# Performance work log

Hardware: AMD Instinct MI355X
Metric: run time of the kernel (lower is better)

## Reference

```python
import jax, jax.numpy as jnp
import numpy as np
import math

IN_CH = 256
RED_CH = 32  # max(256//8, 32)

def setup_inputs() -> dict:
    key = jax.random.key(0)
    k1, k2, k3, k4, k5 = jax.random.split(key, 5)
    x = jax.random.normal(k1, (2, IN_CH, 8, 28, 28), dtype=jnp.float32)
    # 1x1x1 Conv3d weights, kaiming-normal style scale (fan_out)
    def kaiming(k, shape):
        fan_out = shape[0]
        std = math.sqrt(2.0 / fan_out)
        return jax.random.normal(k, shape, dtype=jnp.float32) * std
    q_w = kaiming(k2, (RED_CH, IN_CH))
    k_w = kaiming(k3, (RED_CH, IN_CH))
    v_w = kaiming(k4, (RED_CH, IN_CH))
    out_w = kaiming(k5, (IN_CH, RED_CH))
    return {"x": x, "q_w": q_w, "k_w": k_w, "v_w": v_w, "out_w": out_w}

def reference(x, q_w, k_w, v_w, out_w):
    b, c, t, h, w = x.shape
    n = t * h * w
    xf = x.reshape(b, c, n)  # [B, C, N] (1x1x1 conv == channel matmul)
    q = jnp.einsum('rc,bcn->brn', q_w, xf)  # [B, Cr, N]
    k = jnp.einsum('rc,bcn->brn', k_w, xf)
    v = jnp.einsum('rc,bcn->brn', v_w, xf)
    scale = 1.0 / math.sqrt(RED_CH)
    attn = jnp.einsum('bri,brj->bij', q, k) * scale  # [B, N, N]
    attn = jax.nn.softmax(attn, axis=2)
    out = jnp.einsum('brj,bij->bri', v, attn)  # [B, Cr, N]
    out = jnp.einsum('cr,brn->bcn', out_w, out).reshape(b, c, t, h, w)
    return x + out
```

## Files before the change

### kernel.cpp

```cpp
#include <hip/hip_runtime.h>
#include <hip/hip_bf16.h>

#define NPOS 6272
#define NT   98
#define CIN  256
#define CR   32
#define BATCH 2
#define QS2  0.25503371989518595f
#define PPITCH 72

typedef short bf16x8s __attribute__((ext_vector_type(8)));
typedef short short4v __attribute__((ext_vector_type(4)));
typedef float f32x4   __attribute__((ext_vector_type(4)));
typedef unsigned short ushort_t;

__device__ __forceinline__ ushort_t f2bf(float f) {
    unsigned u = __builtin_bit_cast(unsigned, f);
    u += 0x7fff + ((u >> 16) & 1);
    return (ushort_t)(u >> 16);
}
__device__ __forceinline__ float bf2f(ushort_t h) {
    return __builtin_bit_cast(float, (unsigned)h << 16);
}

__global__ __launch_bounds__(256, 4) void qkv_kernel(
    const float* __restrict__ x, const float* __restrict__ qw,
    const float* __restrict__ kw, const float* __restrict__ vw,
    ushort_t* __restrict__ Qh, ushort_t* __restrict__ Ql,
    ushort_t* __restrict__ Kh, ushort_t* __restrict__ Kl,
    ushort_t* __restrict__ Vt)
{
    const int b   = blockIdx.y;
    const int z   = blockIdx.z;
    const int nl  = threadIdx.x & 63;
    const int n   = blockIdx.x * 64 + nl;
    const int g   = __builtin_amdgcn_readfirstlane(threadIdx.x >> 6);
    const float* w  = (z == 0) ? qw : (z == 1) ? kw : vw;
    const float* wr = w + g * 8 * CIN;
    const float* xb = x + (size_t)b * CIN * NPOS + n;

    float acc[8];
#pragma unroll
    for (int i = 0; i < 8; ++i) acc[i] = 0.f;
#pragma unroll 2
    for (int cb = 0; cb < CIN; cb += 16) {
        float xv[16];
#pragma unroll
        for (int i = 0; i < 16; ++i)
            xv[i] = xb[(size_t)(cb + i) * NPOS];
#pragma unroll
        for (int i = 0; i < 16; ++i)
#pragma unroll
            for (int r = 0; r < 8; ++r)
                acc[r] += wr[r * CIN + cb + i] * xv[i];
    }
    if (z == 2) {
#pragma unroll
        for (int i = 0; i < 8; ++i)
            Vt[((size_t)b * CR + g * 8 + i) * NPOS + n] = f2bf(acc[i]);
    } else {
        ushort_t* dh = (z == 0) ? Qh : Kh;
        ushort_t* dl = (z == 0) ? Ql : Kl;
        float s = (z == 0) ? QS2 : 1.0f;
        bf16x8s fh, fl;
#pragma unroll
        for (int i = 0; i < 8; ++i) {
            float v = acc[i] * s;
            ushort_t h = f2bf(v);
            fh[i] = (short)h;
            fl[i] = (short)f2bf(v - bf2f(h));
        }
        size_t off = ((size_t)b * NPOS + n) * CR + g * 8;
        *(bf16x8s*)(dh + off) = fh;
        *(bf16x8s*)(dl + off) = fl;
    }
}

template <int ITERS>
__global__ __launch_bounds__(128, 3) void attn_kernel(
    const ushort_t* __restrict__ Qh, const ushort_t* __restrict__ Ql,
    const ushort_t* __restrict__ Kh, const ushort_t* __restrict__ Kl,
    const ushort_t* __restrict__ Vt, ushort_t* __restrict__ Opart,
    float* __restrict__ Mp, float* __restrict__ Lp)
{
    __shared__ __align__(16) ushort_t pbuf[2 * 2 * 16 * PPITCH];

    const int lane = threadIdx.x & 63;
    const int wv   = threadIdx.x >> 6;
    const int col  = lane & 15;
    const int quad = lane >> 4;
    const int b    = blockIdx.z;
    const int s    = blockIdx.y;
    const int qw0  = blockIdx.x * 64 + wv * 32;
    ushort_t* pb   = &pbuf[wv * 2 * 16 * PPITCH];

    const ushort_t* Qhb = Qh + (size_t)b * NPOS * CR;
    const ushort_t* Qlb = Ql + (size_t)b * NPOS * CR;
    const ushort_t* Khb = Kh + (size_t)b * NPOS * CR;
    const ushort_t* Klb = Kl + (size_t)b * NPOS * CR;
    const ushort_t* Vtb = Vt + (size_t)b * CR * NPOS;

    bf16x8s qbh[2], qbl[2];
    qbh[0] = *(const bf16x8s*)(Qhb + (size_t)(qw0 + col) * CR + quad * 8);
    qbh[1] = *(const bf16x8s*)(Qhb + (size_t)(qw0 + 16 + col) * CR + quad * 8);
    qbl[0] = *(const bf16x8s*)(Qlb + (size_t)(qw0 + col) * CR + quad * 8);
    qbl[1] = *(const bf16x8s*)(Qlb + (size_t)(qw0 + 16 + col) * CR + quad * 8);

    f32x4 oc[2][2];
#pragma unroll
    for (int h = 0; h < 2; ++h)
#pragma unroll
        for (int c = 0; c < 2; ++c)
#pragma unroll
            for (int r = 0; r < 4; ++r) oc[h][c][r] = 0.f;
    float m_[2] = { -1e30f, -1e30f };
    float l_[2] = { 0.f, 0.f };

#pragma unroll 7
    for (int it = 0; it < ITERS; ++it) {
        const int j0 = (s * ITERS + it) * 64;
        bf16x8s kh[4], kl[4], vb[2][2];
#pragma unroll
        for (int f = 0; f < 4; ++f) {
            kh[f] = *(const bf16x8s*)(Khb + (size_t)(j0 + f * 16 + col) * CR + quad * 8);
            kl[f] = *(const bf16x8s*)(Klb + (size_t)(j0 + f * 16 + col) * CR + quad * 8);
        }
#pragma unroll
        for (int k2 = 0; k2 < 2; ++k2)
#pragma unroll
            for (int c = 0; c < 2; ++c)
                vb[k2][c] = *(const bf16x8s*)(Vtb + (size_t)(c * 16 + col) * NPOS
                                              + j0 + k2 * 32 + quad * 8);

        f32x4 z4; z4[0] = 0.f; z4[1] = 0.f; z4[2] = 0.f; z4[3] = 0.f;
#pragma unroll
        for (int h = 0; h < 2; ++h) {
            f32x4 sc[4];
#pragma unroll
            for (int f = 0; f < 4; ++f) {
                sc[f] = __builtin_amdgcn_mfma_f32_16x16x32_bf16(kl[f], qbh[h], z4, 0, 0, 0);
                sc[f] = __builtin_amdgcn_mfma_f32_16x16x32_bf16(kh[f], qbl[h], sc[f], 0, 0, 0);
                sc[f] = __builtin_amdgcn_mfma_f32_16x16x32_bf16(kh[f], qbh[h], sc[f], 0, 0, 0);
            }
            float v0 = fmaxf(fmaxf(sc[0][0], sc[0][1]), fmaxf(sc[0][2], sc[0][3]));
            float v1 = fmaxf(fmaxf(sc[1][0], sc[1][1]), fmaxf(sc[1][2], sc[1][3]));
            float v2 = fmaxf(fmaxf(sc[2][0], sc[2][1]), fmaxf(sc[2][2], sc[2][3]));
            float v3 = fmaxf(fmaxf(sc[3][0], sc[3][1]), fmaxf(sc[3][2], sc[3][3]));
            float v  = fmaxf(fmaxf(v0, v1), fmaxf(v2, v3));
            v = fmaxf(v, __shfl_xor(v, 16));
            v = fmaxf(v, __shfl_xor(v, 32));
            float mo = m_[h];
            float mn = fmaxf(mo, v);
            float al = __builtin_amdgcn_exp2f(mo - mn);
            float lsum = 0.f;
#pragma unroll
            for (int f = 0; f < 4; ++f) {
                float p0 = __builtin_amdgcn_exp2f(sc[f][0] - mn);
                float p1 = __builtin_amdgcn_exp2f(sc[f][1] - mn);
                float p2 = __builtin_amdgcn_exp2f(sc[f][2] - mn);
                float p3 = __builtin_amdgcn_exp2f(sc[f][3] - mn);
                lsum += (p0 + p1) + (p2 + p3);
                short4v pk;
                pk[0] = (short)f2bf(p0); pk[1] = (short)f2bf(p1);
                pk[2] = (short)f2bf(p2); pk[3] = (short)f2bf(p3);
                *(short4v*)(&pb[h * 16 * PPITCH + col * PPITCH + f * 16 + quad * 4]) = pk;
            }
            m_[h] = mn;
            l_[h] = l_[h] * al + lsum;
#pragma unroll
            for (int r = 0; r < 4; ++r) { oc[h][0][r] *= al; oc[h][1][r] *= al; }
        }
#pragma unroll
        for (int h = 0; h < 2; ++h) {
#pragma unroll
            for (int k2 = 0; k2 < 2; ++k2) {
                bf16x8s pbo = *(const bf16x8s*)(
                    &pb[h * 16 * PPITCH + col * PPITCH + k2 * 32 + quad * 8]);
                oc[h][0] = __builtin_amdgcn_mfma_f32_16x16x32_bf16(vb[k2][0], pbo, oc[h][0], 0, 0, 0);
                oc[h][1] = __builtin_amdgcn_mfma_f32_16x16x32_bf16(vb[k2][1], pbo, oc[h][1], 0, 0, 0);
            }
        }
    }

#pragma unroll
    for (int h = 0; h < 2; ++h) {
        float l = l_[h];
        l += __shfl_xor(l, 16);
        l += __shfl_xor(l, 32);
        l_[h] = l;
    }

    const size_t sb = (size_t)(s * BATCH + b);
    ushort_t* Ob = Opart + sb * CR * NPOS;
#pragma unroll
    for (int h = 0; h < 2; ++h)
#pragma unroll
        for (int c = 0; c < 2; ++c)
#pragma unroll
            for (int r = 0; r < 4; ++r) {
                int ch = c * 16 + quad * 4 + r;
                Ob[(size_t)ch * NPOS + qw0 + h * 16 + col] = f2bf(oc[h][c][r]);
            }
    if (quad == 0) {
#pragma unroll
        for (int h = 0; h < 2; ++h) {
            Mp[sb * NPOS + qw0 + h * 16 + col] = m_[h];
            Lp[sb * NPOS + qw0 + h * 16 + col] = l_[h];
        }
    }
}

template <int S_>
__global__ __launch_bounds__(256) void merge_kernel(
    const ushort_t* __restrict__ Opart, const float* __restrict__ Mp,
    const float* __restrict__ Lp, float* __restrict__ Omrg)
{
    const int b  = blockIdx.y;
    const int z  = blockIdx.z;
    const int nl = threadIdx.x & 63;
    const int n  = blockIdx.x * 64 + nl;
    const int g  = __builtin_amdgcn_readfirstlane(threadIdx.x >> 6);
    const int r  = z * 4 + g;

    float mg = -1e30f;
#pragma unroll
    for (int s = 0; s < S_; ++s)
        mg = fmaxf(mg, Mp[(size_t)(s * BATCH + b) * NPOS + n]);
    float lg = 0.f, acc = 0.f;
#pragma unroll
    for (int s = 0; s < S_; ++s) {
        size_t sb = (size_t)(s * BATCH + b);
        float w = __builtin_amdgcn_exp2f(Mp[sb * NPOS + n] - mg);
        lg  += w * Lp[sb * NPOS + n];
        acc += w * bf2f(Opart[(sb * CR + r) * NPOS + n]);
    }
    Omrg[((size_t)b * CR + r) * NPOS + n] = acc / lg;
}

__global__ __launch_bounds__(256) void proj_kernel(
    const float* __restrict__ Omrg, const float* __restrict__ ow,
    const float* __restrict__ x, float* __restrict__ y)
{
    const int b  = blockIdx.y;
    const int z  = blockIdx.z;
    const int nl = threadIdx.x & 63;
    const int n  = blockIdx.x * 64 + nl;
    const int g  = __builtin_amdgcn_readfirstlane(threadIdx.x >> 6);

    float o[CR];
#pragma unroll
    for (int r = 0; r < CR; ++r)
        o[r] = Omrg[((size_t)b * CR + r) * NPOS + n];

    const float* xb = x + (size_t)b * CIN * NPOS + n;
    float*       yb = y + (size_t)b * CIN * NPOS + n;
    const int c0 = z * 32 + g * 8;
#pragma unroll
    for (int cc = 0; cc < 8; ++cc) {
        int c = c0 + cc;
        float acc = xb[(size_t)c * NPOS];
#pragma unroll
        for (int r = 0; r < CR; ++r) acc += ow[c * CR + r] * o[r];
        yb[(size_t)c * NPOS] = acc;
    }
}

extern "C" void kernel_launch(void* const* d_in, const int* in_sizes, int n_in,
                              void* d_out, int out_size, void* d_ws, size_t ws_size,
                              hipStream_t stream)
{
    const float* x  = (const float*)d_in[0];
    const float* qw = (const float*)d_in[1];
    const float* kw = (const float*)d_in[2];
    const float* vw = (const float*)d_in[3];
    const float* ow = (const float*)d_in[4];
    float* out = (float*)d_out;

    const size_t qkvN = (size_t)BATCH * CR * NPOS;
    const int s_cand[4] = {14, 7, 2, 1};
    int S = 1;
    for (int i = 0; i < 4; ++i) {
        int Sc = s_cand[i];
        size_t need = 5 * qkvN * sizeof(ushort_t)
                    + qkvN * sizeof(float)
                    + (size_t)Sc * qkvN * sizeof(ushort_t)
                    + 2 * (size_t)Sc * BATCH * NPOS * sizeof(float);
        if (need <= ws_size) { S = Sc; break; }
    }
    ushort_t* Qh = (ushort_t*)d_ws;
    ushort_t* Ql = Qh + qkvN;
    ushort_t* Kh = Ql + qkvN;
    ushort_t* Kl = Kh + qkvN;
    ushort_t* Vt = Kl + qkvN;
    float* Omrg  = (float*)(Vt + qkvN);
    ushort_t* Op = (ushort_t*)(Omrg + qkvN);
    float* Mp    = (float*)(Op + (size_t)S * qkvN);
    float* Lp    = Mp + (size_t)S * BATCH * NPOS;

    qkv_kernel<<<dim3(NT, BATCH, 3), 256, 0, stream>>>(x, qw, kw, vw,
                                                       Qh, Ql, Kh, Kl, Vt);
    dim3 ag(NT, S, BATCH);
    switch (S) {
        case 14: attn_kernel<7> <<<ag, 128, 0, stream>>>(Qh, Ql, Kh, Kl, Vt, Op, Mp, Lp); break;
        case 7:  attn_kernel<14><<<ag, 128, 0, stream>>>(Qh, Ql, Kh, Kl, Vt, Op, Mp, Lp); break;
        case 2:  attn_kernel<49><<<ag, 128, 0, stream>>>(Qh, Ql, Kh, Kl, Vt, Op, Mp, Lp); break;
        default: attn_kernel<98><<<ag, 128, 0, stream>>>(Qh, Ql, Kh, Kl, Vt, Op, Mp, Lp); break;
    }
    dim3 mg(NT, BATCH, 8);
    switch (S) {
        case 14: merge_kernel<14><<<mg, 256, 0, stream>>>(Op, Mp, Lp, Omrg); break;
        case 7:  merge_kernel<7> <<<mg, 256, 0, stream>>>(Op, Mp, Lp, Omrg); break;
        case 2:  merge_kernel<2> <<<mg, 256, 0, stream>>>(Op, Mp, Lp, Omrg); break;
        default: merge_kernel<1> <<<mg, 256, 0, stream>>>(Op, Mp, Lp, Omrg); break;
    }
    proj_kernel<<<dim3(NT, BATCH, 8), 256, 0, stream>>>(Omrg, ow, x, out);
}
```

Before: 163.3 us.

## Software-pipeline K/V tile loads in attention loop and simplify QKV projection loop

The attention kernel now prefetches the next K/V tile into registers while computing the current one (double buffering in registers), fully unrolled when ITERS is small. The aim is to hide global-load latency behind the MFMA and softmax work. Launch bounds are relaxed to 2 blocks per SM to make room for the extra registers, which lowers occupancy. The QKV projection loop is also rewritten from 16-channel batches to a single-channel loop unrolled by 8, and its occupancy hint is dropped.

```diff
diff --git a/kernel.cpp b/kernel.cpp
--- a/kernel.cpp
+++ b/kernel.cpp
@@ -23,7 +23,7 @@
     return __builtin_bit_cast(float, (unsigned)h << 16);
 }
 
-__global__ __launch_bounds__(256, 4) void qkv_kernel(
+__global__ __launch_bounds__(256) void qkv_kernel(
     const float* __restrict__ x, const float* __restrict__ qw,
     const float* __restrict__ kw, const float* __restrict__ vw,
     ushort_t* __restrict__ Qh, ushort_t* __restrict__ Ql,
@@ -36,23 +36,17 @@
     const int n   = blockIdx.x * 64 + nl;
     const int g   = __builtin_amdgcn_readfirstlane(threadIdx.x >> 6);
     const float* w  = (z == 0) ? qw : (z == 1) ? kw : vw;
-    const float* wr = w + g * 8 * CIN;
     const float* xb = x + (size_t)b * CIN * NPOS + n;
 
     float acc[8];
 #pragma unroll
     for (int i = 0; i < 8; ++i) acc[i] = 0.f;
-#pragma unroll 2
-    for (int cb = 0; cb < CIN; cb += 16) {
-        float xv[16];
-#pragma unroll
-        for (int i = 0; i < 16; ++i)
-            xv[i] = xb[(size_t)(cb + i) * NPOS];
-#pragma unroll
-        for (int i = 0; i < 16; ++i)
-#pragma unroll
-            for (int r = 0; r < 8; ++r)
-                acc[r] += wr[r * CIN + cb + i] * xv[i];
+#pragma unroll 8
+    for (int c = 0; c < CIN; ++c) {
+        float xv = xb[(size_t)c * NPOS];
+#pragma unroll
+        for (int i = 0; i < 8; ++i)
+            acc[i] += w[(g * 8 + i) * CIN + c] * xv;
     }
     if (z == 2) {
 #pragma unroll
@@ -76,8 +70,82 @@
     }
 }
 
+__device__ __forceinline__ void load_tile(
+    const ushort_t* __restrict__ Khb, const ushort_t* __restrict__ Klb,
+    const ushort_t* __restrict__ Vtb, int j0, int col, int quad,
+    bf16x8s* kh, bf16x8s* kl, bf16x8s* vb)
+{
+#pragma unroll
+    for (int f = 0; f < 4; ++f) {
+        kh[f] = *(const bf16x8s*)(Khb + (size_t)(j0 + f * 16 + col) * CR + quad * 8);
+        kl[f] = *(const bf16x8s*)(Klb + (size_t)(j0 + f * 16 + col) * CR + quad * 8);
+    }
+#pragma unroll
+    for (int k2 = 0; k2 < 2; ++k2)
+#pragma unroll
+        for (int c = 0; c < 2; ++c)
+            vb[k2 * 2 + c] = *(const bf16x8s*)(
+                Vtb + (size_t)(c * 16 + col) * NPOS + j0 + k2 * 32 + quad * 8);
+}
+
+__device__ __forceinline__ void compute_tile(
+    const bf16x8s* kh, const bf16x8s* kl, const bf16x8s* vb,
+    const bf16x8s* qbh, const bf16x8s* qbl,
+    f32x4 (&oc)[2][2], float (&m_)[2], float (&l_)[2],
+    ushort_t* pb, int col, int quad)
+{
+    f32x4 z4 = {0.f, 0.f, 0.f, 0.f};
+#pragma unroll
+    for (int h = 0; h < 2; ++h) {
+        f32x4 sc[4];
+#pragma unroll
+        for (int f = 0; f < 4; ++f) {
+            sc[f] = __builtin_amdgcn_mfma_f32_16x16x32_bf16(kl[f], qbh[h], z4, 0, 0, 0);
+            sc[f] = __builtin_amdgcn_mfma_f32_16x16x32_bf16(kh[f], qbl[h], sc[f], 0, 0, 0);
+            sc[f] = __builtin_amdgcn_mfma_f32_16x16x32_bf16(kh[f], qbh[h], sc[f], 0, 0, 0);
+        }
+        float v0 = fmaxf(fmaxf(sc[0][0], sc[0][1]), fmaxf(sc[0][2], sc[0][3]));
+        float v1 = fmaxf(fmaxf(sc[1][0], sc[1][1]), fmaxf(sc[1][2], sc[1][3]));
+        float v2 = fmaxf(fmaxf(sc[2][0], sc[2][1]), fmaxf(sc[2][2], sc[2][3]));
+        float v3 = fmaxf(fmaxf(sc[3][0], sc[3][1]), fmaxf(sc[3][2], sc[3][3]));
+        float v  = fmaxf(fmaxf(v0, v1), fmaxf(v2, v3));
+        v = fmaxf(v, __shfl_xor(v, 16));
+        v = fmaxf(v, __shfl_xor(v, 32));
+        float mo = m_[h];
+        float mn = fmaxf(mo, v);
+        float al = __builtin_amdgcn_exp2f(mo - mn);
+        float lsum = 0.f;
+#pragma unroll
+        for (int f = 0; f < 4; ++f) {
+            float p0 = __builtin_amdgcn_exp2f(sc[f][0] - mn);
+            float p1 = __builtin_amdgcn_exp2f(sc[f][1] - mn);
+            float p2 = __builtin_amdgcn_exp2f(sc[f][2] - mn);
+            float p3 = __builtin_amdgcn_exp2f(sc[f][3] - mn);
+            lsum += (p0 + p1) + (p2 + p3);
+            short4v pk;
+            pk[0] = (short)f2bf(p0); pk[1] = (short)f2bf(p1);
+            pk[2] = (short)f2bf(p2); pk[3] = (short)f2bf(p3);
+            *(short4v*)(&pb[h * 16 * PPITCH + col * PPITCH + f * 16 + quad * 4]) = pk;
+        }
+        m_[h] = mn;
+        l_[h] = l_[h] * al + lsum;
+#pragma unroll
+        for (int r = 0; r < 4; ++r) { oc[h][0][r] *= al; oc[h][1][r] *= al; }
+    }
+#pragma unroll
+    for (int h = 0; h < 2; ++h) {
+#pragma unroll
+        for (int k2 = 0; k2 < 2; ++k2) {
+            bf16x8s pbo = *(const bf16x8s*)(
+                &pb[h * 16 * PPITCH + col * PPITCH + k2 * 32 + quad * 8]);
+            oc[h][0] = __builtin_amdgcn_mfma_f32_16x16x32_bf16(vb[k2 * 2 + 0], pbo, oc[h][0], 0, 0, 0);
+            oc[h][1] = __builtin_amdgcn_mfma_f32_16x16x32_bf16(vb[k2 * 2 + 1], pbo, oc[h][1], 0, 0, 0);
+        }
+    }
+}
+
 template <int ITERS>
-__global__ __launch_bounds__(128, 3) void attn_kernel(
+__global__ __launch_bounds__(128, 2) void attn_kernel(
     const ushort_t* __restrict__ Qh, const ushort_t* __restrict__ Ql,
     const ushort_t* __restrict__ Kh, const ushort_t* __restrict__ Kl,
     const ushort_t* __restrict__ Vt, ushort_t* __restrict__ Opart,
@@ -116,69 +184,27 @@
     float m_[2] = { -1e30f, -1e30f };
     float l_[2] = { 0.f, 0.f };
 
-#pragma unroll 7
-    for (int it = 0; it < ITERS; ++it) {
-        const int j0 = (s * ITERS + it) * 64;
-        bf16x8s kh[4], kl[4], vb[2][2];
-#pragma unroll
-        for (int f = 0; f < 4; ++f) {
-            kh[f] = *(const bf16x8s*)(Khb + (size_t)(j0 + f * 16 + col) * CR + quad * 8);
-            kl[f] = *(const bf16x8s*)(Klb + (size_t)(j0 + f * 16 + col) * CR + quad * 8);
-        }
-#pragma unroll
-        for (int k2 = 0; k2 < 2; ++k2)
-#pragma unroll
-            for (int c = 0; c < 2; ++c)
-                vb[k2][c] = *(const bf16x8s*)(Vtb + (size_t)(c * 16 + col) * NPOS
-                                              + j0 + k2 * 32 + quad * 8);
-
-        f32x4 z4; z4[0] = 0.f; z4[1] = 0.f; z4[2] = 0.f; z4[3] = 0.f;
-#pragma unroll
-        for (int h = 0; h < 2; ++h) {
-            f32x4 sc[4];
-#pragma unroll
-            for (int f = 0; f < 4; ++f) {
-                sc[f] = __builtin_amdgcn_mfma_f32_16x16x32_bf16(kl[f], qbh[h], z4, 0, 0, 0);
-                sc[f] = __builtin_amdgcn_mfma_f32_16x16x32_bf16(kh[f], qbl[h], sc[f], 0, 0, 0);
-                sc[f] = __builtin_amdgcn_mfma_f32_16x16x32_bf16(kh[f], qbh[h], sc[f], 0, 0, 0);
+    if constexpr (ITERS <= 14) {
+        bf16x8s ckh[4], ckl[4], cvb[4], nkh[4], nkl[4], nvb[4];
+        load_tile(Khb, Klb, Vtb, s * ITERS * 64, col, quad, ckh, ckl, cvb);
+#pragma unroll
+        for (int it = 0; it < ITERS; ++it) {
+            if (it + 1 < ITERS)
+                load_tile(Khb, Klb, Vtb, (s * ITERS + it + 1) * 64, col, quad,
+                          nkh, nkl, nvb);
+            compute_tile(ckh, ckl, cvb, qbh, qbl, oc, m_, l_, pb, col, quad);
+            if (it + 1 < ITERS) {
+#pragma unroll
+                for (int f = 0; f < 4; ++f) {
+                    ckh[f] = nkh[f]; ckl[f] = nkl[f]; cvb[f] = nvb[f];
+                }
             }
-            float v0 = fmaxf(fmaxf(sc[0][0], sc[0][1]), fmaxf(sc[0][2], sc[0][3]));
-            float v1 = fmaxf(fmaxf(sc[1][0], sc[1][1]), fmaxf(sc[1][2], sc[1][3]));
-            float v2 = fmaxf(fmaxf(sc[2][0], sc[2][1]), fmaxf(sc[2][2], sc[2][3]));
-            float v3 = fmaxf(fmaxf(sc[3][0], sc[3][1]), fmaxf(sc[3][2], sc[3][3]));
-            float v  = fmaxf(fmaxf(v0, v1), fmaxf(v2, v3));
-            v = fmaxf(v, __shfl_xor(v, 16));
-            v = fmaxf(v, __shfl_xor(v, 32));
-            float mo = m_[h];
-            float mn = fmaxf(mo, v);
-            float al = __builtin_amdgcn_exp2f(mo - mn);
-            float lsum = 0.f;
-#pragma unroll
-            for (int f = 0; f < 4; ++f) {
-                float p0 = __builtin_amdgcn_exp2f(sc[f][0] - mn);
-                float p1 = __builtin_amdgcn_exp2f(sc[f][1] - mn);
-                float p2 = __builtin_amdgcn_exp2f(sc[f][2] - mn);
-                float p3 = __builtin_amdgcn_exp2f(sc[f][3] - mn);
-                lsum += (p0 + p1) + (p2 + p3);
-                short4v pk;
-                pk[0] = (short)f2bf(p0); pk[1] = (short)f2bf(p1);
-                pk[2] = (short)f2bf(p2); pk[3] = (short)f2bf(p3);
-                *(short4v*)(&pb[h * 16 * PPITCH + col * PPITCH + f * 16 + quad * 4]) = pk;
-            }
-            m_[h] = mn;
-            l_[h] = l_[h] * al + lsum;
-#pragma unroll
-            for (int r = 0; r < 4; ++r) { oc[h][0][r] *= al; oc[h][1][r] *= al; }
-        }
-#pragma unroll
-        for (int h = 0; h < 2; ++h) {
-#pragma unroll
-            for (int k2 = 0; k2 < 2; ++k2) {
-                bf16x8s pbo = *(const bf16x8s*)(
-                    &pb[h * 16 * PPITCH + col * PPITCH + k2 * 32 + quad * 8]);
-                oc[h][0] = __builtin_amdgcn_mfma_f32_16x16x32_bf16(vb[k2][0], pbo, oc[h][0], 0, 0, 0);
-                oc[h][1] = __builtin_amdgcn_mfma_f32_16x16x32_bf16(vb[k2][1], pbo, oc[h][1], 0, 0, 0);
-            }
+        }
+    } else {
+        for (int it = 0; it < ITERS; ++it) {
+            bf16x8s kh[4], kl[4], vb[4];
+            load_tile(Khb, Klb, Vtb, (s * ITERS + it) * 64, col, quad, kh, kl, vb);
+            compute_tile(kh, kl, vb, qbh, qbl, oc, m_, l_, pb, col, quad);
         }
     }
 
```

Measured after the change: 144.3 us. 1.13x faster.
